# Kernel optimization log

Measured on AMD Instinct MI355X. Metric: run time of the kernel, lower is better.

## Reference

```python
import jax, jax.numpy as jnp
import numpy as np
from jax.ops import segment_sum

N = 50000        # nodes
E = 800000       # edges (avg degree 16)
H = 128          # hidden_dim
N_ITER = 2       # BCRefinement n_iterations
TIE_P = 0.05     # fraction of tie (boundary) edges


def setup_inputs() -> dict:
    key = jax.random.key(0)
    ks = jax.random.split(key, 24)
    s = 0.02
    inp = {
        'h': jax.random.normal(ks[0], (N, H), jnp.float32),
        'e': jax.random.normal(ks[1], (E, H), jnp.float32),
        'edge_attr_raw': jax.random.normal(ks[2], (E, 10), jnp.float32),
        # edge_refine: Linear(3H,2H) -> ReLU -> Linear(2H,H)
        'W_er1': s * jax.random.normal(ks[3], (3 * H, 2 * H), jnp.float32),
        'b_er1': jnp.zeros((2 * H,), jnp.float32),
        'W_er2': s * jax.random.normal(ks[4], (2 * H, H), jnp.float32),
        'b_er2': jnp.zeros((H,), jnp.float32),
        # GRUCell(H,H) torch layout: [3H, H] chunks (r, z, n)
        'W_ih': s * jax.random.normal(ks[5], (3 * H, H), jnp.float32),
        'W_hh': s * jax.random.normal(ks[6], (3 * H, H), jnp.float32),
        'b_ih': jnp.zeros((3 * H,), jnp.float32),
        'b_hh': jnp.zeros((3 * H,), jnp.float32),
        # node_neigh_fc: Linear(H,H)
        'W_nn': s * jax.random.normal(ks[7], (H, H), jnp.float32),
        'b_nn': jnp.zeros((H,), jnp.float32),
        # gate_mlp: Linear(3H,H) -> ReLU -> Linear(H,1), last bias init -2.0
        'W_g1': s * jax.random.normal(ks[8], (3 * H, H), jnp.float32),
        'b_g1': jnp.zeros((H,), jnp.float32),
        'W_g2': s * jax.random.normal(ks[9], (H, 1), jnp.float32),
        'b_g2': jnp.full((1,), -2.0, jnp.float32),
        'edge_index': jax.random.randint(ks[10], (2, E), 0, N, jnp.int32),
        'is_tie': jax.random.uniform(ks[11], (E,)) < TIE_P,
    }
    return inp


def reference(h, e, edge_attr_raw,
              W_er1, b_er1, W_er2, b_er2,
              W_ih, W_hh, b_ih, b_hh,
              W_nn, b_nn,
              W_g1, b_g1, W_g2, b_g2,
              edge_index, is_tie):
    row = edge_index[0]
    col = edge_index[1]
    tie_f = is_tie.astype(h.dtype)                        # [E]
    internal = ~is_tie

    # coupling buses: endpoints of any tie edge (tie-incidence count > 0)
    cpl_cnt = segment_sum(tie_f, row, num_segments=N) + \
              segment_sum(tie_f, col, num_segments=N)     # [N]
    is_cpl = cpl_cnt > 0

    # internal edges pointing into coupling buses; b_smooth weights w = 1/sqrt(X^2+eps)
    to_cpl = internal & is_cpl[col]
    X = jnp.abs(edge_attr_raw[:, 1])
    w = jnp.where(to_cpl, 1.0 / jnp.sqrt(X * X + 1e-6), 0.0)
    w_den = segment_sum(w, col, num_segments=N)           # [N]
    w_norm = w / (w_den[col] + 1e-6)                      # [E], zero off-mask

    deg = jnp.maximum(cpl_cnt, 1.0)                       # clamp_min(1.0)

    h_work, e_work = h, e
    for _ in range(N_ITER):
        # --- tie-edge refinement (applied only on tie edges) ---
        edge_in = jnp.concatenate([e_work, h_work[row], h_work[col]], axis=-1)  # [E,3H]
        e_ref = jax.nn.relu(edge_in @ W_er1 + b_er1) @ W_er2 + b_er2            # [E,H]
        e_work = e_work + tie_f[:, None] * e_ref

        # --- node messages from internal neighbors into coupling buses ---
        m_node_msg = h_work[row] @ W_nn + b_nn                                   # [E,H]
        m_node_all = segment_sum(m_node_msg * w_norm[:, None], col,
                                 num_segments=N)                                 # [N,H]

        # --- mean of incident tie-edge features at each node ---
        tie_e = tie_f[:, None] * e_work                                          # [E,H]
        m_edge_all = (segment_sum(tie_e, row, num_segments=N) +
                      segment_sum(tie_e, col, num_segments=N)) / deg[:, None]    # [N,H]

        # --- gating + GRU update on coupling buses ---
        gate_in = jnp.concatenate([m_edge_all, m_node_all, h_work], axis=-1)     # [N,3H]
        gate = jax.nn.sigmoid(jax.nn.relu(gate_in @ W_g1 + b_g1) @ W_g2 + b_g2)  # [N,1]
        m = m_edge_all + gate * m_node_all                                       # [N,H]

        gi = m @ W_ih.T + b_ih                                                   # [N,3H]
        gh = h_work @ W_hh.T + b_hh
        r = jax.nn.sigmoid(gi[:, :H] + gh[:, :H])
        z = jax.nn.sigmoid(gi[:, H:2 * H] + gh[:, H:2 * H])
        n = jnp.tanh(gi[:, 2 * H:] + r * gh[:, 2 * H:])
        h_new = (1.0 - z) * n + z * h_work

        h_work = jnp.where(is_cpl[:, None], h_new, h_work)
    return h_work, e_work
```

## Files before the change

### kernel.cpp

```cpp
#include <hip/hip_runtime.h>
#include <cstdint>

#define N_NODES 50000
#define N_EDGES 800000
#define HDIM    128
#define TIE_CAP 44000
#define NITER   2
#define SCAN_B  256

typedef __attribute__((ext_vector_type(8))) short bf16x8;
typedef __attribute__((ext_vector_type(4))) float f32x4;

__device__ __forceinline__ uint32_t f2bf(float f) {
    uint32_t u = __builtin_bit_cast(uint32_t, f);
    return (u + 0x7fffu + ((u >> 16) & 1u)) >> 16;
}
__device__ __forceinline__ float bf2f(uint32_t b) {
    return __builtin_bit_cast(float, b << 16);
}
__device__ __forceinline__ uint32_t comb2(uint32_t me, uint32_t mn, float g) {
    float a0 = bf2f(me & 0xffffu) + g * bf2f(mn & 0xffffu);
    float a1 = bf2f(me >> 16)     + g * bf2f(mn >> 16);
    return f2bf(a0) | (f2bf(a1) << 16);
}


__device__ __forceinline__ void stage_a128(const float* __restrict__ base,
                                           const int* __restrict__ gidx,
                                           int m0, int Mlim, char* tile, int tid)
{
    const int c = tid & 15;
    #pragma unroll
    for (int p = 0; p < 4; ++p) {
        int row = p * 32 + (tid >> 4);
        int ar = m0 + row; if (ar >= Mlim) ar = Mlim - 1;
        long g = gidx ? gidx[ar] : ar;
        const float* s = base + g * HDIM + c * 4;
        float4 v0 = *(const float4*)s;
        float4 v1 = *(const float4*)(s + 64);
        uint2 w0 = make_uint2(f2bf(v0.x) | (f2bf(v0.y) << 16),
                              f2bf(v0.z) | (f2bf(v0.w) << 16));
        uint2 w1 = make_uint2(f2bf(v1.x) | (f2bf(v1.y) << 16),
                              f2bf(v1.z) | (f2bf(v1.w) << 16));
        int sw = (row & 7) << 4;
        *(uint2*)(tile + row * 256 + ((c * 8) ^ sw)) = w0;
        *(uint2*)(tile + row * 256 + ((c * 8 + 128) ^ sw)) = w1;
    }
}

__device__ __forceinline__ void stage_bf128(const uint16_t* __restrict__ base,
                                            const int* __restrict__ gidx,
                                            int m0, int Mlim, char* tile, int tid)
{
    const int c = tid & 15;
    #pragma unroll
    for (int p = 0; p < 4; ++p) {
        int row = p * 32 + (tid >> 4);
        int ar = m0 + row; if (ar >= Mlim) ar = Mlim - 1;
        long g = gidx ? gidx[ar] : ar;
        uint4 v = *(const uint4*)(base + g * HDIM + c * 8);
        *(uint4*)(tile + row * 256 + ((c * 16) ^ ((row & 7) << 4))) = v;
    }
}

__device__ __forceinline__ void stage_b128(const short* __restrict__ BT, int ldk,
                                           int n0, int k0, char* tile, int tid)
{
    const int c = tid & 15;
    #pragma unroll
    for (int p = 0; p < 4; ++p) {
        int n = p * 32 + (tid >> 4);
        uint4 v = *(const uint4*)&BT[(size_t)(n0 + n) * ldk + k0 + c * 8];
        *(uint4*)(tile + n * 256 + ((c * 16) ^ ((n & 7) << 4))) = v;
    }
}

__device__ __forceinline__ void mfma128(const char* At, const char* Bt,
                                        int wr, int wc, int lane, f32x4 acc[4][2])
{
    #pragma unroll
    for (int ks = 0; ks < 4; ++ks) {
        int kb = ks * 64 + (lane >> 4) * 16;
        bf16x8 aF[4], bF[2];
        #pragma unroll
        for (int mi = 0; mi < 4; ++mi) {
            int row = wr * 64 + mi * 16 + (lane & 15);
            aF[mi] = *(const bf16x8*)(At + row * 256 + (kb ^ ((row & 7) << 4)));
        }
        #pragma unroll
        for (int ni = 0; ni < 2; ++ni) {
            int n = wc * 32 + ni * 16 + (lane & 15);
            bF[ni] = *(const bf16x8*)(Bt + n * 256 + (kb ^ ((n & 7) << 4)));
        }
        #pragma unroll
        for (int mi = 0; mi < 4; ++mi)
            #pragma unroll
            for (int ni = 0; ni < 2; ++ni)
                acc[mi][ni] = __builtin_amdgcn_mfma_f32_16x16x32_bf16(
                    aF[mi], bF[ni], acc[mi][ni], 0, 0, 0);
    }
}

__global__ __launch_bounds__(512)
void k_tie_fused(float* __restrict__ out_e, const uint16_t* __restrict__ h_bf,
                 const int* __restrict__ tie_cnt_p,
                 const int* __restrict__ tie_list, const int* __restrict__ tie_row,
                 const int* __restrict__ tie_col,
                 const short* __restrict__ BTer1, const short* __restrict__ BTer2,
                 const float* __restrict__ b_er1, const float* __restrict__ b_er2,
                 const float* __restrict__ deg_inv, float* __restrict__ m_edge)
{
    int cnt = *tie_cnt_p; if (cnt > TIE_CAP) cnt = TIE_CAP;
    const int m0 = blockIdx.x * 128;
    if (m0 >= cnt) return;

    __shared__ __align__(16) char At[32 * 1024];
    __shared__ __align__(16) char B0[32 * 1024];
    __shared__ __align__(16) char B1[32 * 1024];

    const int tid = threadIdx.x, lane = tid & 63;
    const int wid = tid >> 6, wr = wid >> 2, wc = wid & 3;

    f32x4 acc0[4][2] = {}, acc1[4][2] = {};
    #pragma unroll 1
    for (int c = 0; c < 3; ++c) {
        if (c == 0) stage_a128(out_e, tie_list, m0, cnt, At, tid);
        else        stage_bf128(h_bf, (c == 1) ? tie_row : tie_col, m0, cnt, At, tid);
        stage_b128(BTer1, 384, 0,   c * 128, B0, tid);
        stage_b128(BTer1, 384, 128, c * 128, B1, tid);
        __syncthreads();
        mfma128(At, B0, wr, wc, lane, acc0);
        mfma128(At, B1, wr, wc, lane, acc1);
        __syncthreads();
    }

    #pragma unroll
    for (int half = 0; half < 2; ++half) {
        char* Ct = half ? B0 : At;
        #pragma unroll
        for (int ni = 0; ni < 2; ++ni) {
            int col = wc * 32 + ni * 16 + (lane & 15);
            float bv = b_er1[half * 128 + col];
            #pragma unroll
            for (int mi = 0; mi < 4; ++mi)
                #pragma unroll
                for (int j = 0; j < 4; ++j) {
                    int rl = wr * 64 + mi * 16 + ((lane >> 4) << 2) + j;
                    float v = fmaxf((half ? acc1 : acc0)[mi][ni][j] + bv, 0.f);
                    *(uint16_t*)(Ct + rl * 256 + ((col * 2) ^ ((rl & 7) << 4))) =
                        (uint16_t)f2bf(v);
                }
        }
    }
    stage_b128(BTer2, 256, 0, 0, B1, tid);
    __syncthreads();
    f32x4 acc2[4][2] = {};
    mfma128(At, B1, wr, wc, lane, acc2);
    __syncthreads();
    stage_b128(BTer2, 256, 0, 128, B1, tid);
    __syncthreads();
    mfma128(B0, B1, wr, wc, lane, acc2);

    int col0 = wc * 32 + (lane & 15);
    float bv0 = b_er2[col0], bv1 = b_er2[col0 + 16];
    #pragma unroll
    for (int mi = 0; mi < 4; ++mi) {
        #pragma unroll
        for (int j = 0; j < 4; ++j) {
            int i = m0 + wr * 64 + mi * 16 + ((lane >> 4) << 2) + j;
            if (i < cnt) {
                int e = tie_list[i], r = tie_row[i], cc = tie_col[i];
                float dr = deg_inv[r], dc = deg_inv[cc];
                #pragma unroll
                for (int ni = 0; ni < 2; ++ni) {
                    int col = col0 + ni * 16;
                    float er = acc2[mi][ni][j] + (ni ? bv1 : bv0);
                    size_t eb = (size_t)e * HDIM + col;
                    float v = out_e[eb] + er;
                    out_e[eb] = v;
                    atomicAdd(&m_edge[(size_t)r * HDIM + col], v * dr);
                    atomicAdd(&m_edge[(size_t)cc * HDIM + col], v * dc);
                }
            }
        }
    }
}

__global__ __launch_bounds__(512)
void k_node_mega(const float* __restrict__ m_edge, const uint16_t* __restrict__ agg,
                 float* __restrict__ out_h, uint16_t* __restrict__ h_bf,
                 const float* __restrict__ cpl_cnt, const float* __restrict__ sumw,
                 const short* __restrict__ BTnn, const float* __restrict__ b_nn,
                 const short* __restrict__ BTg1, const float* __restrict__ b_g1,
                 const float* __restrict__ Wg2, const float* __restrict__ b_g2,
                 const short* __restrict__ BTcomb,
                 const short* __restrict__ BTihn, const short* __restrict__ BThhn,
                 const float* __restrict__ b_ih, const float* __restrict__ b_hh)
{
    const int m0 = blockIdx.x * 128;
    __shared__ __align__(16) char Tme[32 * 1024];
    __shared__ __align__(16) char Tmn[32 * 1024];
    __shared__ __align__(16) char Th [32 * 1024];
    __shared__ __align__(16) char Bt [32 * 1024];
    __shared__ float g_red[4][128];
    __shared__ float g_fin[128];
    __shared__ float sw_s[128];

    const int tid = threadIdx.x, lane = tid & 63;
    const int wid = tid >> 6, wr = wid >> 2, wc = wid & 3;

    stage_a128(m_edge, nullptr, m0, N_NODES, Tme, tid);
    stage_bf128(agg,   nullptr, m0, N_NODES, Tmn, tid);
    stage_bf128(h_bf,  nullptr, m0, N_NODES, Th,  tid);
    stage_b128(BTnn, 128, 0, 0, Bt, tid);
    if (tid < 128) {
        int n = m0 + tid; if (n >= N_NODES) n = N_NODES - 1;
        sw_s[tid] = sumw[n];
    }
    __syncthreads();

    {
        f32x4 accM[4][2] = {};
        mfma128(Tmn, Bt, wr, wc, lane, accM);
        __syncthreads();
        #pragma unroll
        for (int ni = 0; ni < 2; ++ni) {
            int col = wc * 32 + ni * 16 + (lane & 15);
            float bv = b_nn[col];
            #pragma unroll
            for (int mi = 0; mi < 4; ++mi)
                #pragma unroll
                for (int j = 0; j < 4; ++j) {
                    int rl = wr * 64 + mi * 16 + ((lane >> 4) << 2) + j;
                    float v = accM[mi][ni][j] + sw_s[rl] * bv;
                    *(uint16_t*)(Tmn + rl * 256 + ((col * 2) ^ ((rl & 7) << 4))) =
                        (uint16_t)f2bf(v);
                }
        }
        __syncthreads();
    }

    f32x4 accG[4][2] = {};
    #pragma unroll 1
    for (int c = 0; c < 3; ++c) {
        const char* Ac = (c == 0) ? Tme : (c == 1) ? Tmn : Th;
        stage_b128(BTg1, 384, 0, c * 128, Bt, tid);
        __syncthreads();
        mfma128(Ac, Bt, wr, wc, lane, accG);
        __syncthreads();
    }
    {
        float bg[2], wg[2];
        #pragma unroll
        for (int ni = 0; ni < 2; ++ni) {
            int col = wc * 32 + ni * 16 + (lane & 15);
            bg[ni] = b_g1[col]; wg[ni] = Wg2[col];
        }
        #pragma unroll
        for (int mi = 0; mi < 4; ++mi)
            #pragma unroll
            for (int j = 0; j < 4; ++j) {
                float p = fmaxf(accG[mi][0][j] + bg[0], 0.f) * wg[0]
                        + fmaxf(accG[mi][1][j] + bg[1], 0.f) * wg[1];
                #pragma unroll
                for (int o = 8; o; o >>= 1) p += __shfl_xor(p, o);
                if ((lane & 15) == 0)
                    g_red[wc][wr * 64 + mi * 16 + ((lane >> 4) << 2) + j] = p;
            }
    }
    __syncthreads();
    if (tid < 128) {
        float t = g_red[0][tid] + g_red[1][tid] + g_red[2][tid] + g_red[3][tid]
                + b_g2[0];
        g_fin[tid] = 1.f / (1.f + __expf(-t));
    }
    __syncthreads();

    {
        const int c = tid & 15;
        #pragma unroll
        for (int p = 0; p < 4; ++p) {
            int row = p * 32 + (tid >> 4);
            float g = g_fin[row];
            int sw = (row & 7) << 4;
            #pragma unroll
            for (int hh = 0; hh < 2; ++hh) {
                int off = (c * 8 + hh * 128) ^ sw;
                uint2 me2 = *(uint2*)(Tme + row * 256 + off);
                uint2 mn2 = *(uint2*)(Tmn + row * 256 + off);
                uint2 o2 = make_uint2(comb2(me2.x, mn2.x, g), comb2(me2.y, mn2.y, g));
                *(uint2*)(Tmn + row * 256 + off) = o2;
            }
        }
    }
    __syncthreads();

    f32x4 aR[4][2] = {}, aZ[4][2] = {}, aGI[4][2] = {}, aGH[4][2] = {};
    stage_b128(BTcomb, 256, 0, 0, Bt, tid);   __syncthreads();
    mfma128(Tmn, Bt, wr, wc, lane, aR);       __syncthreads();
    stage_b128(BTcomb, 256, 0, 128, Bt, tid); __syncthreads();
    mfma128(Th, Bt, wr, wc, lane, aR);        __syncthreads();
    stage_b128(BTcomb, 256, 128, 0, Bt, tid); __syncthreads();
    mfma128(Tmn, Bt, wr, wc, lane, aZ);       __syncthreads();
    stage_b128(BTcomb, 256, 128, 128, Bt, tid); __syncthreads();
    mfma128(Th, Bt, wr, wc, lane, aZ);        __syncthreads();
    stage_b128(BTihn, 128, 0, 0, Bt, tid);    __syncthreads();
    mfma128(Tmn, Bt, wr, wc, lane, aGI);      __syncthreads();
    stage_b128(BThhn, 128, 0, 0, Bt, tid);    __syncthreads();
    mfma128(Th, Bt, wr, wc, lane, aGH);

    #pragma unroll
    for (int ni = 0; ni < 2; ++ni) {
        int col = wc * 32 + ni * 16 + (lane & 15);
        float br  = b_ih[col] + b_hh[col];
        float bz  = b_ih[128 + col] + b_hh[128 + col];
        float bin = b_ih[256 + col], bhn = b_hh[256 + col];
        #pragma unroll
        for (int mi = 0; mi < 4; ++mi)
            #pragma unroll
            for (int j = 0; j < 4; ++j) {
                int node = m0 + wr * 64 + mi * 16 + ((lane >> 4) << 2) + j;
                if (node < N_NODES && cpl_cnt[node] > 0.f) {
                    float r = 1.f / (1.f + __expf(-(aR[mi][ni][j] + br)));
                    float z = 1.f / (1.f + __expf(-(aZ[mi][ni][j] + bz)));
                    float nn = tanhf(aGI[mi][ni][j] + bin + r * (aGH[mi][ni][j] + bhn));
                    size_t hb = (size_t)node * HDIM + col;
                    float hv = out_h[hb];
                    float hn = (1.f - z) * nn + z * hv;
                    out_h[hb] = hn;
                    h_bf[hb] = (uint16_t)f2bf(hn);
                }
            }
    }
}

__global__ __launch_bounds__(256)
void k_mnode_gather(const int* __restrict__ row_ptr, const int* __restrict__ csr_row,
                    const float* __restrict__ csr_w, const uint16_t* __restrict__ h_bf,
                    uint16_t* __restrict__ agg)
{
    int n = blockIdx.x * 4 + (threadIdx.x >> 6);
    if (n >= N_NODES) return;
    int lane = threadIdx.x & 63;
    int s = row_ptr[n], t = row_ptr[n + 1];
    float a0 = 0.f, a1 = 0.f;
    for (int j = s; j < t; ++j) {
        int r = csr_row[j];
        float w = csr_w[j];
        uint32_t v = *(const uint32_t*)(h_bf + (size_t)r * HDIM + lane * 2);
        a0 += w * bf2f(v & 0xffffu);
        a1 += w * bf2f(v >> 16);
    }
    *(uint32_t*)(agg + (size_t)n * HDIM + lane * 2) = f2bf(a0) | (f2bf(a1) << 16);
}

__global__ __launch_bounds__(256)
void k_prepw(const float* __restrict__ W, short* __restrict__ BT,
             int Kd, int Nd, int trans, int total)
{
    int i = blockIdx.x * 256 + threadIdx.x;
    if (i >= total) return;
    int n = i / Kd, k = i % Kd;
    float v = trans ? W[(size_t)k * Nd + n] : W[i];
    BT[i] = (short)f2bf(v);
}

__global__ __launch_bounds__(256)
void k_prepcomb(const float* __restrict__ W_ih, const float* __restrict__ W_hh,
                short* __restrict__ BTcomb)
{
    int i = blockIdx.x * 256 + threadIdx.x;
    if (i >= 256 * 256) return;
    int n = i >> 8, k = i & 255;
    float v = (k < 128) ? W_ih[n * 128 + k] : W_hh[n * 128 + (k - 128)];
    BTcomb[i] = (short)f2bf(v);
}

__global__ __launch_bounds__(256)
void k_h2bf(const float* __restrict__ h, uint16_t* __restrict__ h_bf)
{
    int i = blockIdx.x * 256 + threadIdx.x;
    if (i >= N_NODES * HDIM / 2) return;
    float2 v = *(const float2*)(h + (size_t)i * 2);
    *(uint32_t*)(h_bf + (size_t)i * 2) = f2bf(v.x) | (f2bf(v.y) << 16);
}

__global__ void k_detect(const uint8_t* __restrict__ tie_raw, int* __restrict__ fmt)
{
    __shared__ int cnt;
    if (threadIdx.x == 0) cnt = 0;
    __syncthreads();
    int c = 0;
    for (int i = threadIdx.x; i < 4096; i += 256)
        if ((i & 3) != 0 && tie_raw[i]) c++;
    if (c) atomicAdd(&cnt, c);
    __syncthreads();
    if (threadIdx.x == 0) *fmt = (cnt > 0) ? 1 : 0;
}

__device__ __forceinline__ bool is_tie_e(const void* raw, int fmt, int e)
{
    return fmt ? (((const uint8_t*)raw)[e] != 0) : (((const int*)raw)[e] != 0);
}

__global__ __launch_bounds__(256)
void k_tie(const void* __restrict__ tie_raw, const int* __restrict__ fmt_p,
           const int* __restrict__ ei, float* __restrict__ cpl_cnt,
           int* __restrict__ tie_cnt, int* __restrict__ tie_list,
           int* __restrict__ tie_row, int* __restrict__ tie_col)
{
    int e = blockIdx.x * 256 + threadIdx.x;
    if (e >= N_EDGES) return;
    if (!is_tie_e(tie_raw, *fmt_p, e)) return;
    int r = ei[e], c = ei[N_EDGES + e];
    atomicAdd(&cpl_cnt[r], 1.f);
    atomicAdd(&cpl_cnt[c], 1.f);
    int idx = atomicAdd(tie_cnt, 1);
    if (idx < TIE_CAP) { tie_list[idx] = e; tie_row[idx] = r; tie_col[idx] = c; }
}

__global__ __launch_bounds__(256)
void k_w(const void* __restrict__ tie_raw, const int* __restrict__ fmt_p,
         const int* __restrict__ ei, const float* __restrict__ attr,
         const float* __restrict__ cpl_cnt, float* __restrict__ w_den,
         float* __restrict__ w_arr, int* __restrict__ hist)
{
    int e = blockIdx.x * 256 + threadIdx.x;
    if (e >= N_EDGES) return;
    float w = 0.f;
    if (!is_tie_e(tie_raw, *fmt_p, e)) {
        int c = ei[N_EDGES + e];
        if (cpl_cnt[c] > 0.f) {
            float X = fabsf(attr[(size_t)e * 10 + 1]);
            w = 1.f / sqrtf(X * X + 1e-6f);
            atomicAdd(&w_den[c], w);
            atomicAdd(&hist[c], 1);
        }
    }
    w_arr[e] = w;
}

__global__ __launch_bounds__(256)
void k_wnorm(const int* __restrict__ ei, const float* __restrict__ w_den,
             float* __restrict__ w_arr)
{
    int e = blockIdx.x * 256 + threadIdx.x;
    if (e >= N_EDGES) return;
    float w = w_arr[e];
    if (w != 0.f) {
        int c = ei[N_EDGES + e];
        w_arr[e] = w / (w_den[c] + 1e-6f);
    }
}

__global__ __launch_bounds__(256)
void k_deg(const float* __restrict__ cpl_cnt, const float* __restrict__ w_den,
           float* __restrict__ deg_inv, float* __restrict__ sumw)
{
    int n = blockIdx.x * 256 + threadIdx.x;
    if (n >= N_NODES) return;
    deg_inv[n] = 1.f / fmaxf(cpl_cnt[n], 1.f);
    float wd = w_den[n];
    sumw[n] = wd / (wd + 1e-6f);
}

__global__ __launch_bounds__(SCAN_B)
void k_scan1(const int* __restrict__ cnt, int* __restrict__ excl,
             int* __restrict__ bsum, int n)
{
    __shared__ int s[SCAN_B];
    int t = threadIdx.x;
    int i = blockIdx.x * SCAN_B + t;
    int v = (i < n) ? cnt[i] : 0;
    s[t] = v;
    __syncthreads();
    for (int o = 1; o < SCAN_B; o <<= 1) {
        int u = (t >= o) ? s[t - o] : 0;
        __syncthreads();
        s[t] += u;
        __syncthreads();
    }
    if (i < n) excl[i] = s[t] - v;
    if (t == SCAN_B - 1) bsum[blockIdx.x] = s[t];
}

__global__ void k_scan2(int* __restrict__ bsum, int nb, int* __restrict__ total)
{
    if (threadIdx.x == 0) {
        int run = 0;
        for (int b = 0; b < nb; ++b) { int x = bsum[b]; bsum[b] = run; run += x; }
        *total = run;
    }
}

__global__ __launch_bounds__(256)
void k_scan3(const int* __restrict__ excl, const int* __restrict__ bsum,
             int* __restrict__ row_ptr, int* __restrict__ cursor,
             const int* __restrict__ total, int n)
{
    int i = blockIdx.x * 256 + threadIdx.x;
    if (i < n) {
        int v = excl[i] + bsum[i >> 8];
        row_ptr[i] = v;
        cursor[i] = v;
    }
    if (i == n) row_ptr[n] = *total;
}

__global__ __launch_bounds__(256)
void k_fill(const int* __restrict__ ei, const float* __restrict__ w_arr,
            int* __restrict__ cursor, int* __restrict__ csr_row,
            float* __restrict__ csr_w)
{
    int e = blockIdx.x * 256 + threadIdx.x;
    if (e >= N_EDGES) return;
    float w = w_arr[e];
    if (w == 0.f) return;
    int c = ei[N_EDGES + e];
    int pos = atomicAdd(&cursor[c], 1);
    csr_row[pos] = ei[e];
    csr_w[pos] = w;
}

extern "C" void kernel_launch(void* const* d_in, const int* in_sizes, int n_in,
                              void* d_out, int out_size, void* d_ws, size_t ws_size,
                              hipStream_t stream)
{
    const float* h     = (const float*)d_in[0];
    const float* e     = (const float*)d_in[1];
    const float* attr  = (const float*)d_in[2];
    const float* W_er1 = (const float*)d_in[3];
    const float* b_er1 = (const float*)d_in[4];
    const float* W_er2 = (const float*)d_in[5];
    const float* b_er2 = (const float*)d_in[6];
    const float* W_ih  = (const float*)d_in[7];
    const float* W_hh  = (const float*)d_in[8];
    const float* b_ih  = (const float*)d_in[9];
    const float* b_hh  = (const float*)d_in[10];
    const float* W_nn  = (const float*)d_in[11];
    const float* b_nn  = (const float*)d_in[12];
    const float* W_g1  = (const float*)d_in[13];
    const float* b_g1  = (const float*)d_in[14];
    const float* W_g2  = (const float*)d_in[15];
    const float* b_g2  = (const float*)d_in[16];
    const int*   ei    = (const int*)d_in[17];
    const void*  tie_raw = d_in[18];

    float* out_h = (float*)d_out;
    float* out_e = out_h + (size_t)N_NODES * HDIM;

    char* ws = (char*)d_ws;
    size_t off = 0;
    auto alloc = [&](size_t bytes) -> void* {
        void* p = ws + off;
        off = (off + bytes + 255) & ~(size_t)255;
        return p;
    };
    float* cpl_cnt = (float*)alloc((size_t)N_NODES * 4);
    float* w_den   = (float*)alloc((size_t)N_NODES * 4);
    int*   hist    = (int*)  alloc((size_t)N_NODES * 4);
    int*   counters= (int*)  alloc(256);
    size_t zero_bytes = off;
    float* deg_inv = (float*)alloc((size_t)N_NODES * 4);
    float* sumw    = (float*)alloc((size_t)N_NODES * 4);
    float* w_arr   = (float*)alloc((size_t)N_EDGES * 4);
    int* tie_list  = (int*)alloc((size_t)TIE_CAP * 4);
    int* tie_row   = (int*)alloc((size_t)TIE_CAP * 4);
    int* tie_col   = (int*)alloc((size_t)TIE_CAP * 4);
    short* BTer1   = (short*)alloc((size_t)256 * 384 * 2);
    short* BTer2   = (short*)alloc((size_t)128 * 256 * 2);
    short* BTnn    = (short*)alloc((size_t)128 * 128 * 2);
    short* BTg1    = (short*)alloc((size_t)128 * 384 * 2);
    short* BTcomb  = (short*)alloc((size_t)256 * 256 * 2);
    short* BTihn   = (short*)alloc((size_t)128 * 128 * 2);
    short* BThhn   = (short*)alloc((size_t)128 * 128 * 2);
    uint16_t* h_bf = (uint16_t*)alloc((size_t)N_NODES * HDIM * 2);
    uint16_t* agg  = (uint16_t*)alloc((size_t)N_NODES * HDIM * 2);
    float* m_edge  = (float*)alloc((size_t)N_NODES * HDIM * 4);
    int* excl      = (int*)alloc((size_t)N_NODES * 4);
    int* bsum      = (int*)alloc(256 * 4);
    int* row_ptr   = (int*)alloc((size_t)(N_NODES + 1) * 4);
    int* cursor    = (int*)alloc((size_t)N_NODES * 4);
    int* csr_row   = (int*)alloc((size_t)N_EDGES * 4);
    float* csr_w   = (float*)alloc((size_t)N_EDGES * 4);
    if (off > ws_size) return;

    int* fmt_p     = counters;
    int* tie_cnt   = counters + 1;
    int* csr_total = counters + 2;

    const int EB   = N_EDGES / 256;
    const int GM_T = (TIE_CAP + 127) / 128;
    const int GM_N = (N_NODES + 127) / 128;
    const int NB   = (N_NODES + SCAN_B - 1) / SCAN_B;

    hipMemsetAsync(d_ws, 0, zero_bytes, stream);
    k_detect<<<1, 256, 0, stream>>>((const uint8_t*)tie_raw, fmt_p);
    hipMemcpyAsync(out_h, h, (size_t)N_NODES * HDIM * 4, hipMemcpyDeviceToDevice, stream);
    hipMemcpyAsync(out_e, e, (size_t)N_EDGES * HDIM * 4, hipMemcpyDeviceToDevice, stream);
    k_h2bf<<<(N_NODES * HDIM / 2 + 255) / 256, 256, 0, stream>>>(h, h_bf);

    k_prepw<<<(384*256+255)/256, 256, 0, stream>>>(W_er1, BTer1, 384, 256, 1, 384*256);
    k_prepw<<<(256*128+255)/256, 256, 0, stream>>>(W_er2, BTer2, 256, 128, 1, 256*128);
    k_prepw<<<(128*128+255)/256, 256, 0, stream>>>(W_nn,  BTnn,  128, 128, 1, 128*128);
    k_prepw<<<(384*128+255)/256, 256, 0, stream>>>(W_g1,  BTg1,  384, 128, 1, 384*128);
    k_prepcomb<<<(256*256+255)/256, 256, 0, stream>>>(W_ih, W_hh, BTcomb);
    k_prepw<<<(128*128+255)/256, 256, 0, stream>>>(W_ih + 256*128, BTihn, 128, 128, 0, 128*128);
    k_prepw<<<(128*128+255)/256, 256, 0, stream>>>(W_hh + 256*128, BThhn, 128, 128, 0, 128*128);

    k_tie<<<EB, 256, 0, stream>>>(tie_raw, fmt_p, ei, cpl_cnt, tie_cnt, tie_list, tie_row, tie_col);
    k_w<<<EB, 256, 0, stream>>>(tie_raw, fmt_p, ei, attr, cpl_cnt, w_den, w_arr, hist);
    k_wnorm<<<EB, 256, 0, stream>>>(ei, w_den, w_arr);
    k_deg<<<(N_NODES + 255) / 256, 256, 0, stream>>>(cpl_cnt, w_den, deg_inv, sumw);

    k_scan1<<<NB, SCAN_B, 0, stream>>>(hist, excl, bsum, N_NODES);
    k_scan2<<<1, 64, 0, stream>>>(bsum, NB, csr_total);
    k_scan3<<<(N_NODES + 256) / 256, 256, 0, stream>>>(excl, bsum, row_ptr, cursor, csr_total, N_NODES);
    k_fill<<<EB, 256, 0, stream>>>(ei, w_arr, cursor, csr_row, csr_w);

    for (int it = 0; it < NITER; ++it) {
        hipMemsetAsync(m_edge, 0, (size_t)N_NODES * HDIM * 4, stream);
        k_tie_fused<<<GM_T, 512, 0, stream>>>(
            out_e, h_bf, tie_cnt, tie_list, tie_row, tie_col,
            BTer1, BTer2, b_er1, b_er2, deg_inv, m_edge);
        k_mnode_gather<<<(N_NODES + 3) / 4, 256, 0, stream>>>(row_ptr, csr_row, csr_w, h_bf, agg);
        k_node_mega<<<GM_N, 512, 0, stream>>>(
            m_edge, agg, out_h, h_bf, cpl_cnt, sumw,
            BTnn, b_nn, BTg1, b_g1, W_g2, b_g2,
            BTcomb, BTihn, BThhn, b_ih, b_hh);
    }
}
```

Baseline: 949.4 us.

## Merge all stages into a single cooperative persistent kernel with grid syncs

Replaces the long sequence of small kernel launches, memsets and memcpys with one cooperative kernel of 256 blocks. The blocks loop over tiles for each phase and use grid.sync between phases. The m_edge zeroing moves into the node tile after m_edge has been read, so the separate memset goes away. This targets launch overhead and the idle gaps between the many tiny kernels. In exchange the grid is fixed at 256 blocks of 512 threads, phases with little work still pay for full grid barriers, and occupancy is limited to what fits co-resident.

```diff
diff --git a/kernel.cpp b/kernel.cpp
--- a/kernel.cpp
+++ b/kernel.cpp
@@ -1,15 +1,31 @@
 #include <hip/hip_runtime.h>
+#include <hip/hip_cooperative_groups.h>
 #include <cstdint>
+
+namespace cg = cooperative_groups;
 
 #define N_NODES 50000
 #define N_EDGES 800000
 #define HDIM    128
 #define TIE_CAP 44000
 #define NITER   2
-#define SCAN_B  256
 
 typedef __attribute__((ext_vector_type(8))) short bf16x8;
 typedef __attribute__((ext_vector_type(4))) float f32x4;
+
+struct Params {
+    const float *h, *e, *attr;
+    const float *W_er1, *b_er1, *W_er2, *b_er2;
+    const float *W_ih, *W_hh, *b_ih, *b_hh;
+    const float *W_nn, *b_nn, *W_g1, *b_g1, *W_g2, *b_g2;
+    const int* ei; const void* tie_raw;
+    float *out_h, *out_e;
+    float *cpl_cnt, *w_den, *deg_inv, *sumw, *w_arr, *m_edge, *csr_w;
+    int *hist, *counters, *tie_list, *tie_row, *tie_col;
+    int *excl, *bsum, *row_ptr, *cursor, *csr_row;
+    short *BTer1, *BTer2, *BTnn, *BTg1, *BTcomb, *BTihn, *BThhn;
+    uint16_t *h_bf, *agg;
+};
 
 __device__ __forceinline__ uint32_t f2bf(float f) {
     uint32_t u = __builtin_bit_cast(uint32_t, f);
@@ -23,7 +39,6 @@
     float a1 = bf2f(me >> 16)     + g * bf2f(mn >> 16);
     return f2bf(a0) | (f2bf(a1) << 16);
 }
-
 
 __device__ __forceinline__ void stage_a128(const float* __restrict__ base,
                                            const int* __restrict__ gidx,
@@ -101,46 +116,29 @@
     }
 }
 
-__global__ __launch_bounds__(512)
-void k_tie_fused(float* __restrict__ out_e, const uint16_t* __restrict__ h_bf,
-                 const int* __restrict__ tie_cnt_p,
-                 const int* __restrict__ tie_list, const int* __restrict__ tie_row,
-                 const int* __restrict__ tie_col,
-                 const short* __restrict__ BTer1, const short* __restrict__ BTer2,
-                 const float* __restrict__ b_er1, const float* __restrict__ b_er2,
-                 const float* __restrict__ deg_inv, float* __restrict__ m_edge)
-{
-    int cnt = *tie_cnt_p; if (cnt > TIE_CAP) cnt = TIE_CAP;
-    const int m0 = blockIdx.x * 128;
-    if (m0 >= cnt) return;
-
-    __shared__ __align__(16) char At[32 * 1024];
-    __shared__ __align__(16) char B0[32 * 1024];
-    __shared__ __align__(16) char B1[32 * 1024];
-
-    const int tid = threadIdx.x, lane = tid & 63;
-    const int wid = tid >> 6, wr = wid >> 2, wc = wid & 3;
-
+__device__ __forceinline__ void tie_tile(const Params& P, int m0, int cnt,
+                                         char* At, char* B0, char* B1,
+                                         int tid, int lane, int wr, int wc)
+{
     f32x4 acc0[4][2] = {}, acc1[4][2] = {};
     #pragma unroll 1
     for (int c = 0; c < 3; ++c) {
-        if (c == 0) stage_a128(out_e, tie_list, m0, cnt, At, tid);
-        else        stage_bf128(h_bf, (c == 1) ? tie_row : tie_col, m0, cnt, At, tid);
-        stage_b128(BTer1, 384, 0,   c * 128, B0, tid);
-        stage_b128(BTer1, 384, 128, c * 128, B1, tid);
+        if (c == 0) stage_a128(P.out_e, P.tie_list, m0, cnt, At, tid);
+        else        stage_bf128(P.h_bf, (c == 1) ? P.tie_row : P.tie_col, m0, cnt, At, tid);
+        stage_b128(P.BTer1, 384, 0,   c * 128, B0, tid);
+        stage_b128(P.BTer1, 384, 128, c * 128, B1, tid);
         __syncthreads();
         mfma128(At, B0, wr, wc, lane, acc0);
         mfma128(At, B1, wr, wc, lane, acc1);
         __syncthreads();
     }
-
     #pragma unroll
     for (int half = 0; half < 2; ++half) {
         char* Ct = half ? B0 : At;
         #pragma unroll
         for (int ni = 0; ni < 2; ++ni) {
             int col = wc * 32 + ni * 16 + (lane & 15);
-            float bv = b_er1[half * 128 + col];
+            float bv = P.b_er1[half * 128 + col];
             #pragma unroll
             for (int mi = 0; mi < 4; ++mi)
                 #pragma unroll
@@ -152,72 +150,61 @@
                 }
         }
     }
-    stage_b128(BTer2, 256, 0, 0, B1, tid);
+    stage_b128(P.BTer2, 256, 0, 0, B1, tid);
     __syncthreads();
     f32x4 acc2[4][2] = {};
     mfma128(At, B1, wr, wc, lane, acc2);
     __syncthreads();
-    stage_b128(BTer2, 256, 0, 128, B1, tid);
+    stage_b128(P.BTer2, 256, 0, 128, B1, tid);
     __syncthreads();
     mfma128(B0, B1, wr, wc, lane, acc2);
 
     int col0 = wc * 32 + (lane & 15);
-    float bv0 = b_er2[col0], bv1 = b_er2[col0 + 16];
+    float bv0 = P.b_er2[col0], bv1 = P.b_er2[col0 + 16];
     #pragma unroll
     for (int mi = 0; mi < 4; ++mi) {
         #pragma unroll
         for (int j = 0; j < 4; ++j) {
             int i = m0 + wr * 64 + mi * 16 + ((lane >> 4) << 2) + j;
             if (i < cnt) {
-                int e = tie_list[i], r = tie_row[i], cc = tie_col[i];
-                float dr = deg_inv[r], dc = deg_inv[cc];
+                int e = P.tie_list[i], r = P.tie_row[i], cc = P.tie_col[i];
+                float dr = P.deg_inv[r], dc = P.deg_inv[cc];
                 #pragma unroll
                 for (int ni = 0; ni < 2; ++ni) {
                     int col = col0 + ni * 16;
                     float er = acc2[mi][ni][j] + (ni ? bv1 : bv0);
                     size_t eb = (size_t)e * HDIM + col;
-                    float v = out_e[eb] + er;
-                    out_e[eb] = v;
-                    atomicAdd(&m_edge[(size_t)r * HDIM + col], v * dr);
-                    atomicAdd(&m_edge[(size_t)cc * HDIM + col], v * dc);
+                    float v = P.out_e[eb] + er;
+                    P.out_e[eb] = v;
+                    atomicAdd(&P.m_edge[(size_t)r * HDIM + col], v * dr);
+                    atomicAdd(&P.m_edge[(size_t)cc * HDIM + col], v * dc);
                 }
             }
         }
     }
 }
 
-__global__ __launch_bounds__(512)
-void k_node_mega(const float* __restrict__ m_edge, const uint16_t* __restrict__ agg,
-                 float* __restrict__ out_h, uint16_t* __restrict__ h_bf,
-                 const float* __restrict__ cpl_cnt, const float* __restrict__ sumw,
-                 const short* __restrict__ BTnn, const float* __restrict__ b_nn,
-                 const short* __restrict__ BTg1, const float* __restrict__ b_g1,
-                 const float* __restrict__ Wg2, const float* __restrict__ b_g2,
-                 const short* __restrict__ BTcomb,
-                 const short* __restrict__ BTihn, const short* __restrict__ BThhn,
-                 const float* __restrict__ b_ih, const float* __restrict__ b_hh)
-{
-    const int m0 = blockIdx.x * 128;
-    __shared__ __align__(16) char Tme[32 * 1024];
-    __shared__ __align__(16) char Tmn[32 * 1024];
-    __shared__ __align__(16) char Th [32 * 1024];
-    __shared__ __align__(16) char Bt [32 * 1024];
-    __shared__ float g_red[4][128];
-    __shared__ float g_fin[128];
-    __shared__ float sw_s[128];
-
-    const int tid = threadIdx.x, lane = tid & 63;
-    const int wid = tid >> 6, wr = wid >> 2, wc = wid & 3;
-
-    stage_a128(m_edge, nullptr, m0, N_NODES, Tme, tid);
-    stage_bf128(agg,   nullptr, m0, N_NODES, Tmn, tid);
-    stage_bf128(h_bf,  nullptr, m0, N_NODES, Th,  tid);
-    stage_b128(BTnn, 128, 0, 0, Bt, tid);
+__device__ __forceinline__ void mega_tile(const Params& P, int m0,
+                                          char* Tme, char* Tmn, char* Th, char* Bt,
+                                          float (&g_red)[4][128], float* g_fin,
+                                          float* sw_s,
+                                          int tid, int lane, int wr, int wc)
+{
+    stage_a128(P.m_edge, nullptr, m0, N_NODES, Tme, tid);
+    stage_bf128(P.agg,   nullptr, m0, N_NODES, Tmn, tid);
+    stage_bf128(P.h_bf,  nullptr, m0, N_NODES, Th,  tid);
+    stage_b128(P.BTnn, 128, 0, 0, Bt, tid);
     if (tid < 128) {
         int n = m0 + tid; if (n >= N_NODES) n = N_NODES - 1;
-        sw_s[tid] = sumw[n];
-    }
-    __syncthreads();
+        sw_s[tid] = P.sumw[n];
+    }
+    __syncthreads();
+
+    {
+        int lim = (N_NODES - m0 < 128 ? N_NODES - m0 : 128) * HDIM / 4;
+        float4* mp = (float4*)(P.m_edge + (size_t)m0 * HDIM);
+        for (int i = tid; i < lim; i += 512) mp[i] = make_float4(0.f, 0.f, 0.f, 0.f);
+    }
 
     {
         f32x4 accM[4][2] = {};
@@ -226,7 +213,7 @@
         #pragma unroll
         for (int ni = 0; ni < 2; ++ni) {
             int col = wc * 32 + ni * 16 + (lane & 15);
-            float bv = b_nn[col];
+            float bv = P.b_nn[col];
             #pragma unroll
             for (int mi = 0; mi < 4; ++mi)
                 #pragma unroll
@@ -244,7 +231,7 @@
     #pragma unroll 1
     for (int c = 0; c < 3; ++c) {
         const char* Ac = (c == 0) ? Tme : (c == 1) ? Tmn : Th;
-        stage_b128(BTg1, 384, 0, c * 128, Bt, tid);
+        stage_b128(P.BTg1, 384, 0, c * 128, Bt, tid);
         __syncthreads();
         mfma128(Ac, Bt, wr, wc, lane, accG);
         __syncthreads();
@@ -254,7 +241,7 @@
         #pragma unroll
         for (int ni = 0; ni < 2; ++ni) {
             int col = wc * 32 + ni * 16 + (lane & 15);
-            bg[ni] = b_g1[col]; wg[ni] = Wg2[col];
+            bg[ni] = P.b_g1[col]; wg[ni] = P.W_g2[col];
         }
         #pragma unroll
         for (int mi = 0; mi < 4; ++mi)
@@ -271,7 +258,7 @@
     __syncthreads();
     if (tid < 128) {
         float t = g_red[0][tid] + g_red[1][tid] + g_red[2][tid] + g_red[3][tid]
-                + b_g2[0];
+                + P.b_g2[0];
         g_fin[tid] = 1.f / (1.f + __expf(-t));
     }
     __syncthreads();
@@ -296,258 +283,243 @@
     __syncthreads();
 
     f32x4 aR[4][2] = {}, aZ[4][2] = {}, aGI[4][2] = {}, aGH[4][2] = {};
-    stage_b128(BTcomb, 256, 0, 0, Bt, tid);   __syncthreads();
-    mfma128(Tmn, Bt, wr, wc, lane, aR);       __syncthreads();
-    stage_b128(BTcomb, 256, 0, 128, Bt, tid); __syncthreads();
-    mfma128(Th, Bt, wr, wc, lane, aR);        __syncthreads();
-    stage_b128(BTcomb, 256, 128, 0, Bt, tid); __syncthreads();
-    mfma128(Tmn, Bt, wr, wc, lane, aZ);       __syncthreads();
-    stage_b128(BTcomb, 256, 128, 128, Bt, tid); __syncthreads();
-    mfma128(Th, Bt, wr, wc, lane, aZ);        __syncthreads();
-    stage_b128(BTihn, 128, 0, 0, Bt, tid);    __syncthreads();
-    mfma128(Tmn, Bt, wr, wc, lane, aGI);      __syncthreads();
-    stage_b128(BThhn, 128, 0, 0, Bt, tid);    __syncthreads();
+    stage_b128(P.BTcomb, 256, 0, 0, Bt, tid);     __syncthreads();
+    mfma128(Tmn, Bt, wr, wc, lane, aR);           __syncthreads();
+    stage_b128(P.BTcomb, 256, 0, 128, Bt, tid);   __syncthreads();
+    mfma128(Th, Bt, wr, wc, lane, aR);            __syncthreads();
+    stage_b128(P.BTcomb, 256, 128, 0, Bt, tid);   __syncthreads();
+    mfma128(Tmn, Bt, wr, wc, lane, aZ);           __syncthreads();
+    stage_b128(P.BTcomb, 256, 128, 128, Bt, tid); __syncthreads();
+    mfma128(Th, Bt, wr, wc, lane, aZ);            __syncthreads();
+    stage_b128(P.BTihn, 128, 0, 0, Bt, tid);      __syncthreads();
+    mfma128(Tmn, Bt, wr, wc, lane, aGI);          __syncthreads();
+    stage_b128(P.BThhn, 128, 0, 0, Bt, tid);      __syncthreads();
     mfma128(Th, Bt, wr, wc, lane, aGH);
 
     #pragma unroll
     for (int ni = 0; ni < 2; ++ni) {
         int col = wc * 32 + ni * 16 + (lane & 15);
-        float br  = b_ih[col] + b_hh[col];
-        float bz  = b_ih[128 + col] + b_hh[128 + col];
-        float bin = b_ih[256 + col], bhn = b_hh[256 + col];
+        float br  = P.b_ih[col] + P.b_hh[col];
+        float bz  = P.b_ih[128 + col] + P.b_hh[128 + col];
+        float bin = P.b_ih[256 + col], bhn = P.b_hh[256 + col];
         #pragma unroll
         for (int mi = 0; mi < 4; ++mi)
             #pragma unroll
             for (int j = 0; j < 4; ++j) {
                 int node = m0 + wr * 64 + mi * 16 + ((lane >> 4) << 2) + j;
-                if (node < N_NODES && cpl_cnt[node] > 0.f) {
+                if (node < N_NODES && P.cpl_cnt[node] > 0.f) {
                     float r = 1.f / (1.f + __expf(-(aR[mi][ni][j] + br)));
                     float z = 1.f / (1.f + __expf(-(aZ[mi][ni][j] + bz)));
                     float nn = tanhf(aGI[mi][ni][j] + bin + r * (aGH[mi][ni][j] + bhn));
                     size_t hb = (size_t)node * HDIM + col;
-                    float hv = out_h[hb];
+                    float hv = P.out_h[hb];
                     float hn = (1.f - z) * nn + z * hv;
-                    out_h[hb] = hn;
-                    h_bf[hb] = (uint16_t)f2bf(hn);
+                    P.out_h[hb] = hn;
+                    P.h_bf[hb] = (uint16_t)f2bf(hn);
                 }
             }
     }
 }
 
-__global__ __launch_bounds__(256)
-void k_mnode_gather(const int* __restrict__ row_ptr, const int* __restrict__ csr_row,
-                    const float* __restrict__ csr_w, const uint16_t* __restrict__ h_bf,
-                    uint16_t* __restrict__ agg)
-{
-    int n = blockIdx.x * 4 + (threadIdx.x >> 6);
-    if (n >= N_NODES) return;
-    int lane = threadIdx.x & 63;
-    int s = row_ptr[n], t = row_ptr[n + 1];
-    float a0 = 0.f, a1 = 0.f;
-    for (int j = s; j < t; ++j) {
-        int r = csr_row[j];
-        float w = csr_w[j];
-        uint32_t v = *(const uint32_t*)(h_bf + (size_t)r * HDIM + lane * 2);
-        a0 += w * bf2f(v & 0xffffu);
-        a1 += w * bf2f(v >> 16);
-    }
-    *(uint32_t*)(agg + (size_t)n * HDIM + lane * 2) = f2bf(a0) | (f2bf(a1) << 16);
-}
-
-__global__ __launch_bounds__(256)
-void k_prepw(const float* __restrict__ W, short* __restrict__ BT,
-             int Kd, int Nd, int trans, int total)
-{
-    int i = blockIdx.x * 256 + threadIdx.x;
-    if (i >= total) return;
-    int n = i / Kd, k = i % Kd;
-    float v = trans ? W[(size_t)k * Nd + n] : W[i];
-    BT[i] = (short)f2bf(v);
-}
-
-__global__ __launch_bounds__(256)
-void k_prepcomb(const float* __restrict__ W_ih, const float* __restrict__ W_hh,
-                short* __restrict__ BTcomb)
-{
-    int i = blockIdx.x * 256 + threadIdx.x;
-    if (i >= 256 * 256) return;
-    int n = i >> 8, k = i & 255;
-    float v = (k < 128) ? W_ih[n * 128 + k] : W_hh[n * 128 + (k - 128)];
-    BTcomb[i] = (short)f2bf(v);
-}
-
-__global__ __launch_bounds__(256)
-void k_h2bf(const float* __restrict__ h, uint16_t* __restrict__ h_bf)
-{
-    int i = blockIdx.x * 256 + threadIdx.x;
-    if (i >= N_NODES * HDIM / 2) return;
-    float2 v = *(const float2*)(h + (size_t)i * 2);
-    *(uint32_t*)(h_bf + (size_t)i * 2) = f2bf(v.x) | (f2bf(v.y) << 16);
-}
-
-__global__ void k_detect(const uint8_t* __restrict__ tie_raw, int* __restrict__ fmt)
-{
-    __shared__ int cnt;
-    if (threadIdx.x == 0) cnt = 0;
-    __syncthreads();
-    int c = 0;
-    for (int i = threadIdx.x; i < 4096; i += 256)
-        if ((i & 3) != 0 && tie_raw[i]) c++;
-    if (c) atomicAdd(&cnt, c);
-    __syncthreads();
-    if (threadIdx.x == 0) *fmt = (cnt > 0) ? 1 : 0;
-}
-
-__device__ __forceinline__ bool is_tie_e(const void* raw, int fmt, int e)
-{
-    return fmt ? (((const uint8_t*)raw)[e] != 0) : (((const int*)raw)[e] != 0);
-}
-
-__global__ __launch_bounds__(256)
-void k_tie(const void* __restrict__ tie_raw, const int* __restrict__ fmt_p,
-           const int* __restrict__ ei, float* __restrict__ cpl_cnt,
-           int* __restrict__ tie_cnt, int* __restrict__ tie_list,
-           int* __restrict__ tie_row, int* __restrict__ tie_col)
-{
-    int e = blockIdx.x * 256 + threadIdx.x;
-    if (e >= N_EDGES) return;
-    if (!is_tie_e(tie_raw, *fmt_p, e)) return;
-    int r = ei[e], c = ei[N_EDGES + e];
-    atomicAdd(&cpl_cnt[r], 1.f);
-    atomicAdd(&cpl_cnt[c], 1.f);
-    int idx = atomicAdd(tie_cnt, 1);
-    if (idx < TIE_CAP) { tie_list[idx] = e; tie_row[idx] = r; tie_col[idx] = c; }
-}
-
-__global__ __launch_bounds__(256)
-void k_w(const void* __restrict__ tie_raw, const int* __restrict__ fmt_p,
-         const int* __restrict__ ei, const float* __restrict__ attr,
-         const float* __restrict__ cpl_cnt, float* __restrict__ w_den,
-         float* __restrict__ w_arr, int* __restrict__ hist)
-{
-    int e = blockIdx.x * 256 + threadIdx.x;
-    if (e >= N_EDGES) return;
-    float w = 0.f;
-    if (!is_tie_e(tie_raw, *fmt_p, e)) {
-        int c = ei[N_EDGES + e];
-        if (cpl_cnt[c] > 0.f) {
-            float X = fabsf(attr[(size_t)e * 10 + 1]);
-            w = 1.f / sqrtf(X * X + 1e-6f);
-            atomicAdd(&w_den[c], w);
-            atomicAdd(&hist[c], 1);
-        }
-    }
-    w_arr[e] = w;
-}
-
-__global__ __launch_bounds__(256)
-void k_wnorm(const int* __restrict__ ei, const float* __restrict__ w_den,
-             float* __restrict__ w_arr)
-{
-    int e = blockIdx.x * 256 + threadIdx.x;
-    if (e >= N_EDGES) return;
-    float w = w_arr[e];
-    if (w != 0.f) {
-        int c = ei[N_EDGES + e];
-        w_arr[e] = w / (w_den[c] + 1e-6f);
-    }
-}
-
-__global__ __launch_bounds__(256)
-void k_deg(const float* __restrict__ cpl_cnt, const float* __restrict__ w_den,
-           float* __restrict__ deg_inv, float* __restrict__ sumw)
-{
-    int n = blockIdx.x * 256 + threadIdx.x;
-    if (n >= N_NODES) return;
-    deg_inv[n] = 1.f / fmaxf(cpl_cnt[n], 1.f);
-    float wd = w_den[n];
-    sumw[n] = wd / (wd + 1e-6f);
-}
-
-__global__ __launch_bounds__(SCAN_B)
-void k_scan1(const int* __restrict__ cnt, int* __restrict__ excl,
-             int* __restrict__ bsum, int n)
-{
-    __shared__ int s[SCAN_B];
-    int t = threadIdx.x;
-    int i = blockIdx.x * SCAN_B + t;
-    int v = (i < n) ? cnt[i] : 0;
-    s[t] = v;
-    __syncthreads();
-    for (int o = 1; o < SCAN_B; o <<= 1) {
-        int u = (t >= o) ? s[t - o] : 0;
-        __syncthreads();
-        s[t] += u;
-        __syncthreads();
-    }
-    if (i < n) excl[i] = s[t] - v;
-    if (t == SCAN_B - 1) bsum[blockIdx.x] = s[t];
-}
-
-__global__ void k_scan2(int* __restrict__ bsum, int nb, int* __restrict__ total)
-{
-    if (threadIdx.x == 0) {
+__global__ __launch_bounds__(512)
+void k_mono(Params P)
+{
+    cg::grid_group grid = cg::this_grid();
+    __shared__ __align__(16) char S0[32 * 1024];
+    __shared__ __align__(16) char S1[32 * 1024];
+    __shared__ __align__(16) char S2[32 * 1024];
+    __shared__ __align__(16) char S3[32 * 1024];
+    __shared__ float g_red[4][128];
+    __shared__ float g_fin[128];
+    __shared__ float sw_s[128];
+    __shared__ int   scan_s[512];
+
+    const int tid = threadIdx.x, bid = blockIdx.x;
+    const int lane = tid & 63, wid = tid >> 6, wr = wid >> 2, wc = wid & 3;
+    const int nb = gridDim.x;
+    const int gtid = bid * 512 + tid, gstr = nb * 512;
+
+    if (bid == 0 && tid < 64) {
+        const uint8_t* tr = (const uint8_t*)P.tie_raw;
+        int c = 0;
+        for (int i = tid; i < 4096; i += 64)
+            if ((i & 3) && tr[i]) c = 1;
+        unsigned long long m = __ballot(c != 0);
+        if (tid == 0) { P.counters[0] = (m != 0ull) ? 1 : 0; P.counters[1] = 0; P.counters[2] = 0; }
+    }
+    for (int i = gtid; i < N_NODES * HDIM / 4; i += gstr) {
+        float4 v = ((const float4*)P.h)[i];
+        ((float4*)P.out_h)[i] = v;
+        uint2 w = make_uint2(f2bf(v.x) | (f2bf(v.y) << 16),
+                             f2bf(v.z) | (f2bf(v.w) << 16));
+        *(uint2*)(P.h_bf + (size_t)i * 4) = w;
+    }
+    for (int i = gtid; i < N_EDGES * HDIM / 4; i += gstr)
+        ((float4*)P.out_e)[i] = ((const float4*)P.e)[i];
+    for (int i = gtid; i < N_NODES; i += gstr) {
+        P.cpl_cnt[i] = 0.f; P.w_den[i] = 0.f; P.hist[i] = 0;
+    }
+    for (int i = gtid; i < N_NODES * HDIM / 4; i += gstr)
+        ((float4*)P.m_edge)[i] = make_float4(0.f, 0.f, 0.f, 0.f);
+    for (int i = gtid; i < 384 * 256; i += gstr) { int n = i / 384, k = i % 384; P.BTer1[i] = (short)f2bf(P.W_er1[(size_t)k * 256 + n]); }
+    for (int i = gtid; i < 128 * 256; i += gstr) { int n = i / 256, k = i % 256; P.BTer2[i] = (short)f2bf(P.W_er2[(size_t)k * 128 + n]); }
+    for (int i = gtid; i < 128 * 128; i += gstr) { int n = i / 128, k = i % 128; P.BTnn[i]  = (short)f2bf(P.W_nn [(size_t)k * 128 + n]); }
+    for (int i = gtid; i < 128 * 384; i += gstr) { int n = i / 384, k = i % 384; P.BTg1[i]  = (short)f2bf(P.W_g1 [(size_t)k * 128 + n]); }
+    for (int i = gtid; i < 256 * 256; i += gstr) { int n = i >> 8, k = i & 255; float v = (k < 128) ? P.W_ih[n * 128 + k] : P.W_hh[n * 128 + (k - 128)]; P.BTcomb[i] = (short)f2bf(v); }
+    for (int i = gtid; i < 128 * 128; i += gstr) { P.BTihn[i] = (short)f2bf(P.W_ih[256 * 128 + i]); P.BThhn[i] = (short)f2bf(P.W_hh[256 * 128 + i]); }
+    grid.sync();
+
+    {
+        int fmt = P.counters[0];
+        for (int e = gtid; e < N_EDGES; e += gstr) {
+            bool t = fmt ? (((const uint8_t*)P.tie_raw)[e] != 0)
+                         : (((const int*)P.tie_raw)[e] != 0);
+            if (t) {
+                int r = P.ei[e], c = P.ei[N_EDGES + e];
+                atomicAdd(&P.cpl_cnt[r], 1.f);
+                atomicAdd(&P.cpl_cnt[c], 1.f);
+                int idx = atomicAdd(&P.counters[1], 1);
+                if (idx < TIE_CAP) { P.tie_list[idx] = e; P.tie_row[idx] = r; P.tie_col[idx] = c; }
+            }
+        }
+    }
+    grid.sync();
+
+    {
+        int fmt = P.counters[0];
+        for (int e = gtid; e < N_EDGES; e += gstr) {
+            bool t = fmt ? (((const uint8_t*)P.tie_raw)[e] != 0)
+                         : (((const int*)P.tie_raw)[e] != 0);
+            float w = 0.f;
+            if (!t) {
+                int c = P.ei[N_EDGES + e];
+                if (P.cpl_cnt[c] > 0.f) {
+                    float X = fabsf(P.attr[(size_t)e * 10 + 1]);
+                    w = 1.f / sqrtf(X * X + 1e-6f);
+                    atomicAdd(&P.w_den[c], w);
+                    atomicAdd(&P.hist[c], 1);
+                }
+            }
+            P.w_arr[e] = w;
+        }
+    }
+    grid.sync();
+
+    for (int e = gtid; e < N_EDGES; e += gstr) {
+        float w = P.w_arr[e];
+        if (w != 0.f) P.w_arr[e] = w / (P.w_den[P.ei[N_EDGES + e]] + 1e-6f);
+    }
+    for (int n = gtid; n < N_NODES; n += gstr) {
+        P.deg_inv[n] = 1.f / fmaxf(P.cpl_cnt[n], 1.f);
+        float wd = P.w_den[n];
+        P.sumw[n] = wd / (wd + 1e-6f);
+    }
+    const int NCH = (N_NODES + 511) / 512;
+    for (int vb = bid; vb < NCH; vb += nb) {
+        int i = vb * 512 + tid;
+        int v = (i < N_NODES) ? P.hist[i] : 0;
+        scan_s[tid] = v;
+        __syncthreads();
+        for (int o = 1; o < 512; o <<= 1) {
+            int u = (tid >= o) ? scan_s[tid - o] : 0;
+            __syncthreads();
+            scan_s[tid] += u;
+            __syncthreads();
+        }
+        if (i < N_NODES) P.excl[i] = scan_s[tid] - v;
+        if (tid == 511) P.bsum[vb] = scan_s[tid];
+        __syncthreads();
+    }
+    grid.sync();
+
+    if (bid == 0 && tid == 0) {
         int run = 0;
-        for (int b = 0; b < nb; ++b) { int x = bsum[b]; bsum[b] = run; run += x; }
-        *total = run;
-    }
-}
-
-__global__ __launch_bounds__(256)
-void k_scan3(const int* __restrict__ excl, const int* __restrict__ bsum,
-             int* __restrict__ row_ptr, int* __restrict__ cursor,
-             const int* __restrict__ total, int n)
-{
-    int i = blockIdx.x * 256 + threadIdx.x;
-    if (i < n) {
-        int v = excl[i] + bsum[i >> 8];
-        row_ptr[i] = v;
-        cursor[i] = v;
-    }
-    if (i == n) row_ptr[n] = *total;
-}
-
-__global__ __launch_bounds__(256)
-void k_fill(const int* __restrict__ ei, const float* __restrict__ w_arr,
-            int* __restrict__ cursor, int* __restrict__ csr_row,
-            float* __restrict__ csr_w)
-{
-    int e = blockIdx.x * 256 + threadIdx.x;
-    if (e >= N_EDGES) return;
-    float w = w_arr[e];
-    if (w == 0.f) return;
-    int c = ei[N_EDGES + e];
-    int pos = atomicAdd(&cursor[c], 1);
-    csr_row[pos] = ei[e];
-    csr_w[pos] = w;
+        for (int b = 0; b < NCH; ++b) { int x = P.bsum[b]; P.bsum[b] = run; run += x; }
+        P.counters[2] = run;
+    }
+    grid.sync();
+
+    for (int i = gtid; i < N_NODES; i += gstr) {
+        int v = P.excl[i] + P.bsum[i >> 9];
+        P.row_ptr[i] = v;
+        P.cursor[i] = v;
+    }
+    if (gtid == 0) P.row_ptr[N_NODES] = P.counters[2];
+    grid.sync();
+
+    for (int e = gtid; e < N_EDGES; e += gstr) {
+        float w = P.w_arr[e];
+        if (w != 0.f) {
+            int c = P.ei[N_EDGES + e];
+            int pos = atomicAdd(&P.cursor[c], 1);
+            P.csr_row[pos] = P.ei[e];
+            P.csr_w[pos] = w;
+        }
+    }
+    grid.sync();
+
+    int cnt = P.counters[1]; if (cnt > TIE_CAP) cnt = TIE_CAP;
+    const int ntt = (cnt + 127) / 128;
+    const int ntn = (N_NODES + 127) / 128;
+
+    for (int it = 0; it < NITER; ++it) {
+        for (int t = bid; t < ntt; t += nb) {
+            __syncthreads();
+            tie_tile(P, t * 128, cnt, S0, S1, S2, tid, lane, wr, wc);
+        }
+        {
+            int wv = bid * 8 + wid;
+            for (int n = wv; n < N_NODES; n += nb * 8) {
+                int s = P.row_ptr[n], t2 = P.row_ptr[n + 1];
+                float a0 = 0.f, a1 = 0.f;
+                for (int j = s; j < t2; ++j) {
+                    int r = P.csr_row[j];
+                    float w = P.csr_w[j];
+                    uint32_t v = *(const uint32_t*)(P.h_bf + (size_t)r * HDIM + lane * 2);
+                    a0 += w * bf2f(v & 0xffffu);
+                    a1 += w * bf2f(v >> 16);
+                }
+                *(uint32_t*)(P.agg + (size_t)n * HDIM + lane * 2) =
+                    f2bf(a0) | (f2bf(a1) << 16);
+            }
+        }
+        grid.sync();
+        for (int t = bid; t < ntn; t += nb) {
+            __syncthreads();
+            mega_tile(P, t * 128, S0, S1, S2, S3, g_red, g_fin, sw_s,
+                      tid, lane, wr, wc);
+        }
+        grid.sync();
+    }
 }
 
 extern "C" void kernel_launch(void* const* d_in, const int* in_sizes, int n_in,
                               void* d_out, int out_size, void* d_ws, size_t ws_size,
                               hipStream_t stream)
 {
-    const float* h     = (const float*)d_in[0];
-    const float* e     = (const float*)d_in[1];
-    const float* attr  = (const float*)d_in[2];
-    const float* W_er1 = (const float*)d_in[3];
-    const float* b_er1 = (const float*)d_in[4];
-    const float* W_er2 = (const float*)d_in[5];
-    const float* b_er2 = (const float*)d_in[6];
-    const float* W_ih  = (const float*)d_in[7];
-    const float* W_hh  = (const float*)d_in[8];
-    const float* b_ih  = (const float*)d_in[9];
-    const float* b_hh  = (const float*)d_in[10];
-    const float* W_nn  = (const float*)d_in[11];
-    const float* b_nn  = (const float*)d_in[12];
-    const float* W_g1  = (const float*)d_in[13];
-    const float* b_g1  = (const float*)d_in[14];
-    const float* W_g2  = (const float*)d_in[15];
-    const float* b_g2  = (const float*)d_in[16];
-    const int*   ei    = (const int*)d_in[17];
-    const void*  tie_raw = d_in[18];
-
-    float* out_h = (float*)d_out;
-    float* out_e = out_h + (size_t)N_NODES * HDIM;
+    Params P;
+    P.h     = (const float*)d_in[0];
+    P.e     = (const float*)d_in[1];
+    P.attr  = (const float*)d_in[2];
+    P.W_er1 = (const float*)d_in[3];
+    P.b_er1 = (const float*)d_in[4];
+    P.W_er2 = (const float*)d_in[5];
+    P.b_er2 = (const float*)d_in[6];
+    P.W_ih  = (const float*)d_in[7];
+    P.W_hh  = (const float*)d_in[8];
+    P.b_ih  = (const float*)d_in[9];
+    P.b_hh  = (const float*)d_in[10];
+    P.W_nn  = (const float*)d_in[11];
+    P.b_nn  = (const float*)d_in[12];
+    P.W_g1  = (const float*)d_in[13];
+    P.b_g1  = (const float*)d_in[14];
+    P.W_g2  = (const float*)d_in[15];
+    P.b_g2  = (const float*)d_in[16];
+    P.ei    = (const int*)d_in[17];
+    P.tie_raw = d_in[18];
+
+    P.out_h = (float*)d_out;
+    P.out_e = P.out_h + (size_t)N_NODES * HDIM;
 
     char* ws = (char*)d_ws;
     size_t off = 0;
@@ -556,77 +528,34 @@
         off = (off + bytes + 255) & ~(size_t)255;
         return p;
     };
-    float* cpl_cnt = (float*)alloc((size_t)N_NODES * 4);
-    float* w_den   = (float*)alloc((size_t)N_NODES * 4);
-    int*   hist    = (int*)  alloc((size_t)N_NODES * 4);
-    int*   counters= (int*)  alloc(256);
-    size_t zero_bytes = off;
-    float* deg_inv = (float*)alloc((size_t)N_NODES * 4);
-    float* sumw    = (float*)alloc((size_t)N_NODES * 4);
-    float* w_arr   = (float*)alloc((size_t)N_EDGES * 4);
-    int* tie_list  = (int*)alloc((size_t)TIE_CAP * 4);
-    int* tie_row   = (int*)alloc((size_t)TIE_CAP * 4);
-    int* tie_col   = (int*)alloc((size_t)TIE_CAP * 4);
-    short* BTer1   = (short*)alloc((size_t)256 * 384 * 2);
-    short* BTer2   = (short*)alloc((size_t)128 * 256 * 2);
-    short* BTnn    = (short*)alloc((size_t)128 * 128 * 2);
-    short* BTg1    = (short*)alloc((size_t)128 * 384 * 2);
-    short* BTcomb  = (short*)alloc((size_t)256 * 256 * 2);
-    short* BTihn   = (short*)alloc((size_t)128 * 128 * 2);
-    short* BThhn   = (short*)alloc((size_t)128 * 128 * 2);
-    uint16_t* h_bf = (uint16_t*)alloc((size_t)N_NODES * HDIM * 2);
-    uint16_t* agg  = (uint16_t*)alloc((size_t)N_NODES * HDIM * 2);
-    float* m_edge  = (float*)alloc((size_t)N_NODES * HDIM * 4);
-    int* excl      = (int*)alloc((size_t)N_NODES * 4);
-    int* bsum      = (int*)alloc(256 * 4);
-    int* row_ptr   = (int*)alloc((size_t)(N_NODES + 1) * 4);
-    int* cursor    = (int*)alloc((size_t)N_NODES * 4);
-    int* csr_row   = (int*)alloc((size_t)N_EDGES * 4);
-    float* csr_w   = (float*)alloc((size_t)N_EDGES * 4);
+    P.cpl_cnt = (float*)alloc((size_t)N_NODES * 4);
+    P.w_den   = (float*)alloc((size_t)N_NODES * 4);
+    P.hist    = (int*)  alloc((size_t)N_NODES * 4);
+    P.counters= (int*)  alloc(256);
+    P.deg_inv = (float*)alloc((size_t)N_NODES * 4);
+    P.sumw    = (float*)alloc((size_t)N_NODES * 4);
+    P.w_arr   = (float*)alloc((size_t)N_EDGES * 4);
+    P.tie_list= (int*)alloc((size_t)TIE_CAP * 4);
+    P.tie_row = (int*)alloc((size_t)TIE_CAP * 4);
+    P.tie_col = (int*)alloc((size_t)TIE_CAP * 4);
+    P.BTer1   = (short*)alloc((size_t)256 * 384 * 2);
+    P.BTer2   = (short*)alloc((size_t)128 * 256 * 2);
+    P.BTnn    = (short*)alloc((size_t)128 * 128 * 2);
+    P.BTg1    = (short*)alloc((size_t)128 * 384 * 2);
+    P.BTcomb  = (short*)alloc((size_t)256 * 256 * 2);
+    P.BTihn   = (short*)alloc((size_t)128 * 128 * 2);
+    P.BThhn   = (short*)alloc((size_t)128 * 128 * 2);
+    P.h_bf    = (uint16_t*)alloc((size_t)N_NODES * HDIM * 2);
+    P.agg     = (uint16_t*)alloc((size_t)N_NODES * HDIM * 2);
+    P.m_edge  = (float*)alloc((size_t)N_NODES * HDIM * 4);
+    P.excl    = (int*)alloc((size_t)N_NODES * 4);
+    P.bsum    = (int*)alloc(256 * 4);
+    P.row_ptr = (int*)alloc((size_t)(N_NODES + 1) * 4);
+    P.cursor  = (int*)alloc((size_t)N_NODES * 4);
+    P.csr_row = (int*)alloc((size_t)N_EDGES * 4);
+    P.csr_w   = (float*)alloc((size_t)N_EDGES * 4);
     if (off > ws_size) return;
 
-    int* fmt_p     = counters;
-    int* tie_cnt   = counters + 1;
-    int* csr_total = counters + 2;
-
-    const int EB   = N_EDGES / 256;
-    const int GM_T = (TIE_CAP + 127) / 128;
-    const int GM_N = (N_NODES + 127) / 128;
-    const int NB   = (N_NODES + SCAN_B - 1) / SCAN_B;
-
-    hipMemsetAsync(d_ws, 0, zero_bytes, stream);
-    k_detect<<<1, 256, 0, stream>>>((const uint8_t*)tie_raw, fmt_p);
-    hipMemcpyAsync(out_h, h, (size_t)N_NODES * HDIM * 4, hipMemcpyDeviceToDevice, stream);
-    hipMemcpyAsync(out_e, e, (size_t)N_EDGES * HDIM * 4, hipMemcpyDeviceToDevice, stream);
-    k_h2bf<<<(N_NODES * HDIM / 2 + 255) / 256, 256, 0, stream>>>(h, h_bf);
-
-    k_prepw<<<(384*256+255)/256, 256, 0, stream>>>(W_er1, BTer1, 384, 256, 1, 384*256);
-    k_prepw<<<(256*128+255)/256, 256, 0, stream>>>(W_er2, BTer2, 256, 128, 1, 256*128);
-    k_prepw<<<(128*128+255)/256, 256, 0, stream>>>(W_nn,  BTnn,  128, 128, 1, 128*128);
-    k_prepw<<<(384*128+255)/256, 256, 0, stream>>>(W_g1,  BTg1,  384, 128, 1, 384*128);
-    k_prepcomb<<<(256*256+255)/256, 256, 0, stream>>>(W_ih, W_hh, BTcomb);
-    k_prepw<<<(128*128+255)/256, 256, 0, stream>>>(W_ih + 256*128, BTihn, 128, 128, 0, 128*128);
-    k_prepw<<<(128*128+255)/256, 256, 0, stream>>>(W_hh + 256*128, BThhn, 128, 128, 0, 128*128);
-
-    k_tie<<<EB, 256, 0, stream>>>(tie_raw, fmt_p, ei, cpl_cnt, tie_cnt, tie_list, tie_row, tie_col);
-    k_w<<<EB, 256, 0, stream>>>(tie_raw, fmt_p, ei, attr, cpl_cnt, w_den, w_arr, hist);
-    k_wnorm<<<EB, 256, 0, stream>>>(ei, w_den, w_arr);
-    k_deg<<<(N_NODES + 255) / 256, 256, 0, stream>>>(cpl_cnt, w_den, deg_inv, sumw);
-
-    k_scan1<<<NB, SCAN_B, 0, stream>>>(hist, excl, bsum, N_NODES);
-    k_scan2<<<1, 64, 0, stream>>>(bsum, NB, csr_total);
-    k_scan3<<<(N_NODES + 256) / 256, 256, 0, stream>>>(excl, bsum, row_ptr, cursor, csr_total, N_NODES);
-    k_fill<<<EB, 256, 0, stream>>>(ei, w_arr, cursor, csr_row, csr_w);
-
-    for (int it = 0; it < NITER; ++it) {
-        hipMemsetAsync(m_edge, 0, (size_t)N_NODES * HDIM * 4, stream);
-        k_tie_fused<<<GM_T, 512, 0, stream>>>(
-            out_e, h_bf, tie_cnt, tie_list, tie_row, tie_col,
-            BTer1, BTer2, b_er1, b_er2, deg_inv, m_edge);
-        k_mnode_gather<<<(N_NODES + 3) / 4, 256, 0, stream>>>(row_ptr, csr_row, csr_w, h_bf, agg);
-        k_node_mega<<<GM_N, 512, 0, stream>>>(
-            m_edge, agg, out_h, h_bf, cpl_cnt, sumw,
-            BTnn, b_nn, BTg1, b_g1, W_g2, b_g2,
-            BTcomb, BTihn, BThhn, b_ih, b_hh);
-    }
-}
+    void* args[] = { &P };
+    hipLaunchCooperativeKernel((void*)k_mono, dim3(256), dim3(512), args, 0, stream);
+}
```

Result: slower. 1.585 ms (+67.0%).
